# Performance work log

Measured on AMD Instinct MI355X. Metric: run time of the kernel, lower is better.

## Reference

```python
import jax, jax.numpy as jnp
import numpy as np

H = 256
VOCAB = 32000
B = 128
T = 2048


def setup_inputs() -> dict:
    key = jax.random.key(0)
    ks = jax.random.split(key, 14)
    s = 0.05
    return {
        "tokens": jax.random.randint(ks[0], (B, 1), 0, VOCAB),
        "hidden": jax.random.normal(ks[1], (1, B, H), jnp.float32),
        "encoder_outputs": jax.random.normal(ks[2], (T, B, H), jnp.float32),
        "emb_table": jax.random.normal(ks[3], (VOCAB + 1, H), jnp.float32) * s,
        "attn_W": jax.random.normal(ks[4], (1, 2 * H), jnp.float32) * s,
        "attn_b": jax.random.normal(ks[5], (1,), jnp.float32) * s,
        "comb_W": jax.random.normal(ks[6], (H, 2 * H), jnp.float32) * s,
        "comb_b": jax.random.normal(ks[7], (H,), jnp.float32) * s,
        "gru_Wih": jax.random.normal(ks[8], (3 * H, H), jnp.float32) * s,
        "gru_Whh": jax.random.normal(ks[9], (3 * H, H), jnp.float32) * s,
        "gru_bih": jax.random.normal(ks[10], (3 * H,), jnp.float32) * s,
        "gru_bhh": jax.random.normal(ks[11], (3 * H,), jnp.float32) * s,
        "out_W": jax.random.normal(ks[12], (VOCAB, H), jnp.float32) * s,
        "out_b": jax.random.normal(ks[13], (VOCAB,), jnp.float32) * s,
    }


def reference(tokens, hidden, encoder_outputs, emb_table, attn_W, attn_b,
              comb_W, comb_b, gru_Wih, gru_Whh, gru_bih, gru_bhh, out_W, out_b):
    h = hidden.shape[-1]
    # Embedding lookup: [B,1] -> [B,1,H] -> [1,B,H]
    emb = jnp.transpose(emb_table[tokens], (1, 0, 2))
    # Additive attention: Linear([hidden; enc_t]) -> scalar score per position.
    # attn_W splits into hidden part (first H cols) and encoder part (last H).
    W_h, W_e = attn_W[:, :h], attn_W[:, h:]          # [1,H] each
    scores = (jnp.einsum('tbh,oh->tbo', encoder_outputs, W_e)
              + jnp.einsum('lbh,oh->lbo', hidden, W_h)  # broadcast over T
              + attn_b)                                  # [T,B,1]
    attn_w = jax.nn.softmax(scores, axis=0)              # softmax over time
    # Context: weighted sum over time -> [1,B,H]
    ctx = jnp.einsum('tbo,tbh->obh', attn_w, encoder_outputs)
    # Combine embedded input with context, relu
    x = jnp.concatenate([emb, ctx], axis=2)              # [1,B,2H]
    x = jax.nn.relu(jnp.einsum('lbk,hk->lbh', x, comb_W) + comb_b)  # [1,B,H]
    # Single GRU step (PyTorch gate ordering: r, z, n)
    gx = x[0] @ gru_Wih.T + gru_bih                      # [B,3H]
    gh = hidden[0] @ gru_Whh.T + gru_bhh                 # [B,3H]
    r = jax.nn.sigmoid(gx[:, :h] + gh[:, :h])
    z = jax.nn.sigmoid(gx[:, h:2 * h] + gh[:, h:2 * h])
    n = jnp.tanh(gx[:, 2 * h:] + r * gh[:, 2 * h:])
    h_new = ((1.0 - z) * n + z * hidden[0])[None]        # [1,B,H]
    # Output projection + log_softmax over vocab
    logits = jnp.einsum('lbh,vh->lbv', h_new, out_W) + out_b
    logp = jax.nn.log_softmax(logits, axis=2)            # [1,B,V]
    return (logp, h_new, jnp.transpose(attn_w, (1, 0, 2)), ctx)
```

## Files before the change

### kernel.cpp

```cpp
#include <hip/hip_runtime.h>
#include <cstddef>

constexpr int H  = 256;
constexpr int Bb = 128;
constexpr int T  = 2048;
constexpr int V  = 32000;
constexpr int SPLITS = 16;
constexpr int TC = T / SPLITS;
constexpr int NPART = SPLITS * 4;
constexpr int LSE_SPLIT = 4;
constexpr int VS = V / LSE_SPLIT;

typedef __attribute__((ext_vector_type(8))) short short8;
typedef __attribute__((ext_vector_type(4))) float f32x4;

__device__ __forceinline__ unsigned short bf1(float a) {
  unsigned u = __builtin_bit_cast(unsigned, a);
  return (unsigned short)((u + 0x7fffu + ((u >> 16) & 1u)) >> 16);
}
__device__ __forceinline__ unsigned bfpack2(float a, float b) {
  unsigned ua = __builtin_bit_cast(unsigned, a);
  unsigned ub = __builtin_bit_cast(unsigned, b);
  ua = (ua + 0x7fffu + ((ua >> 16) & 1u)) >> 16;
  ub = (ub + 0x7fffu + ((ub >> 16) & 1u)) & 0xffff0000u;
  return ua | ub;
}

__global__ __launch_bounds__(256) void k_attn(
    const float* __restrict__ enc, const float* __restrict__ hidden,
    const float* __restrict__ attn_W, const float* __restrict__ attn_b,
    float* __restrict__ scores, float* __restrict__ ctx_part) {
  const int b = blockIdx.y, chunk = blockIdx.x;
  const int tid = threadIdx.x, lane = tid & 63, wave = tid >> 6;

  const float4 we = *(const float4*)(attn_W + H + lane * 4);
  const float4 wh = *(const float4*)(attn_W + lane * 4);
  const float4 hv = *(const float4*)(hidden + (size_t)b * H + lane * 4);

  float hb = fmaf(wh.x, hv.x, fmaf(wh.y, hv.y, fmaf(wh.z, hv.z, wh.w * hv.w)));
  #pragma unroll
  for (int off = 1; off < 64; off <<= 1) hb += __shfl_xor(hb, off);
  hb += attn_b[0];

  const int t0 = chunk * TC + wave * 32;
  const float* base = enc + (size_t)t0 * (Bb * H) + (size_t)b * H + lane * 4;

  float4 acc = {0.f, 0.f, 0.f, 0.f};
  for (int i = 0; i < 32; i += 4) {
    float4 e0 = *(const float4*)(base + (size_t)(i + 0) * (Bb * H));
    float4 e1 = *(const float4*)(base + (size_t)(i + 1) * (Bb * H));
    float4 e2 = *(const float4*)(base + (size_t)(i + 2) * (Bb * H));
    float4 e3 = *(const float4*)(base + (size_t)(i + 3) * (Bb * H));

    float p0 = fmaf(e0.x, we.x, fmaf(e0.y, we.y, fmaf(e0.z, we.z, e0.w * we.w)));
    float p1 = fmaf(e1.x, we.x, fmaf(e1.y, we.y, fmaf(e1.z, we.z, e1.w * we.w)));
    float p2 = fmaf(e2.x, we.x, fmaf(e2.y, we.y, fmaf(e2.z, we.z, e2.w * we.w)));
    float p3 = fmaf(e3.x, we.x, fmaf(e3.y, we.y, fmaf(e3.z, we.z, e3.w * we.w)));
    #pragma unroll
    for (int off = 1; off < 64; off <<= 1) {
      p0 += __shfl_xor(p0, off);
      p1 += __shfl_xor(p1, off);
      p2 += __shfl_xor(p2, off);
      p3 += __shfl_xor(p3, off);
    }
    float s0 = p0 + hb, s1 = p1 + hb, s2 = p2 + hb, s3 = p3 + hb;
    float w0 = __expf(s0), w1 = __expf(s1), w2 = __expf(s2), w3 = __expf(s3);

    acc.x = fmaf(w0, e0.x, fmaf(w1, e1.x, fmaf(w2, e2.x, fmaf(w3, e3.x, acc.x))));
    acc.y = fmaf(w0, e0.y, fmaf(w1, e1.y, fmaf(w2, e2.y, fmaf(w3, e3.y, acc.y))));
    acc.z = fmaf(w0, e0.z, fmaf(w1, e1.z, fmaf(w2, e2.z, fmaf(w3, e3.z, acc.z))));
    acc.w = fmaf(w0, e0.w, fmaf(w1, e1.w, fmaf(w2, e2.w, fmaf(w3, e3.w, acc.w))));

    if (lane == 0) {
      float4 sv = {s0, s1, s2, s3};
      *(float4*)(scores + (size_t)b * T + t0 + i) = sv;
    }
  }
  float* cp = ctx_part + ((size_t)b * NPART + chunk * 4 + wave) * H + lane * 4;
  *(float4*)cp = acc;
}

__global__ __launch_bounds__(256) void k_softmax_ctx(
    const float* __restrict__ scores, const float* __restrict__ ctx_part,
    float* __restrict__ attn_o, float* __restrict__ ctx_o) {
  const int b = blockIdx.x, tid = threadIdx.x;
  const int lane = tid & 63, wave = tid >> 6;
  __shared__ float red[4];
  __shared__ float m_sh, l_sh;

  const float* sb = scores + (size_t)b * T;
  float s[8];
  #pragma unroll
  for (int q = 0; q < 8; q++) s[q] = sb[tid + 256 * q];

  float mx = s[0];
  #pragma unroll
  for (int q = 1; q < 8; q++) mx = fmaxf(mx, s[q]);
  #pragma unroll
  for (int off = 1; off < 64; off <<= 1) mx = fmaxf(mx, __shfl_xor(mx, off));
  if (lane == 0) red[wave] = mx;
  __syncthreads();
  if (tid == 0) m_sh = fmaxf(fmaxf(red[0], red[1]), fmaxf(red[2], red[3]));
  __syncthreads();
  const float m = m_sh;

  float w[8];
  float ps = 0.f;
  #pragma unroll
  for (int q = 0; q < 8; q++) { w[q] = __expf(s[q] - m); ps += w[q]; }
  #pragma unroll
  for (int off = 1; off < 64; off <<= 1) ps += __shfl_xor(ps, off);
  __syncthreads();
  if (lane == 0) red[wave] = ps;
  __syncthreads();
  if (tid == 0) l_sh = red[0] + red[1] + red[2] + red[3];
  __syncthreads();
  const float inv = 1.f / l_sh;

  #pragma unroll
  for (int q = 0; q < 8; q++) attn_o[(size_t)b * T + tid + 256 * q] = w[q] * inv;

  float c = 0.f;
  for (int si = 0; si < NPART; si++)
    c += ctx_part[((size_t)b * NPART + si) * H + tid];
  ctx_o[(size_t)b * H + tid] = c * __expf(-m) * inv;
}

__global__ __launch_bounds__(256) void k_comb_gru(
    const int* __restrict__ tokens, const float* __restrict__ hidden,
    const float* __restrict__ emb_table,
    const float* __restrict__ comb_W, const float* __restrict__ comb_b,
    const float* __restrict__ Wih, const float* __restrict__ Whh,
    const float* __restrict__ bih, const float* __restrict__ bhh,
    const float* __restrict__ ctx_o, float* __restrict__ hnew,
    unsigned short* __restrict__ hnewb) {
  const int b = blockIdx.x, tid = threadIdx.x;
  __shared__ __align__(16) float x2[2 * H];
  __shared__ __align__(16) float hid[H];
  __shared__ __align__(16) float xs[H];

  const int tok = tokens[b];
  x2[tid]     = emb_table[(size_t)tok * H + tid];
  x2[H + tid] = ctx_o[(size_t)b * H + tid];
  hid[tid]    = hidden[(size_t)b * H + tid];
  __syncthreads();

  {
    const float4* wr = (const float4*)(comb_W + (size_t)tid * (2 * H));
    const float4* xr = (const float4*)x2;
    float a = 0.f;
    #pragma unroll 8
    for (int k = 0; k < (2 * H) / 4; k++) {
      float4 w = wr[k], x = xr[k];
      a += w.x * x.x + w.y * x.y + w.z * x.z + w.w * x.w;
    }
    a += comb_b[tid];
    xs[tid] = fmaxf(a, 0.f);
  }
  __syncthreads();

  auto dot256 = [](const float* __restrict__ row, const float* __restrict__ v) -> float {
    const float4* r4 = (const float4*)row;
    const float4* v4 = (const float4*)v;
    float a = 0.f;
    #pragma unroll 8
    for (int k = 0; k < H / 4; k++) {
      float4 w = r4[k], x = v4[k];
      a += w.x * x.x + w.y * x.y + w.z * x.z + w.w * x.w;
    }
    return a;
  };

  float gxr = dot256(Wih + (size_t)tid * H,           xs) + bih[tid];
  float gxz = dot256(Wih + (size_t)(tid + H) * H,     xs) + bih[tid + H];
  float gxn = dot256(Wih + (size_t)(tid + 2 * H) * H, xs) + bih[tid + 2 * H];
  float ghr = dot256(Whh + (size_t)tid * H,           hid) + bhh[tid];
  float ghz = dot256(Whh + (size_t)(tid + H) * H,     hid) + bhh[tid + H];
  float ghn = dot256(Whh + (size_t)(tid + 2 * H) * H, hid) + bhh[tid + 2 * H];

  float r = 1.f / (1.f + __expf(-(gxr + ghr)));
  float z = 1.f / (1.f + __expf(-(gxz + ghz)));
  float n = tanhf(gxn + r * ghn);
  float hv = (1.f - z) * n + z * hid[tid];
  hnew[(size_t)b * H + tid] = hv;
  hnewb[(size_t)b * H + tid] = bf1(hv);
}

constexpr int LSTR = 72;
__global__ __launch_bounds__(256) void k_logits(
    const unsigned short* __restrict__ hnewb, const float* __restrict__ out_W,
    const float* __restrict__ out_b, float* __restrict__ logits) {
  const int tid = threadIdx.x;
  const int lane = tid & 63, wave = tid >> 6;
  const int v0 = blockIdx.x * 128;
  const int r16 = lane & 15, quad = lane >> 4;

  __shared__ __align__(16) short lA[128 * LSTR];
  __shared__ __align__(16) short lB[128 * LSTR];

  f32x4 acc[8][2];
  #pragma unroll
  for (int mt = 0; mt < 8; mt++) {
    acc[mt][0] = (f32x4){0.f, 0.f, 0.f, 0.f};
    acc[mt][1] = (f32x4){0.f, 0.f, 0.f, 0.f};
  }

  for (int k0 = 0; k0 < H; k0 += 64) {
    #pragma unroll
    for (int q = 0; q < 4; q++) {
      int idx = q * 256 + tid;
      int row = idx >> 3, c8 = idx & 7;
      f32x4 v = *(const f32x4*)(hnewb + (size_t)row * H + k0 + c8 * 8);
      *(f32x4*)(&lA[row * LSTR + c8 * 8]) = v;
    }
    #pragma unroll
    for (int q = 0; q < 8; q++) {
      int idx = q * 256 + tid;
      int row = idx >> 4, c4 = idx & 15;
      f32x4 wv = *(const f32x4*)(out_W + (size_t)(v0 + row) * H + k0 + c4 * 4);
      uint2 p;
      p.x = bfpack2(wv.x, wv.y);
      p.y = bfpack2(wv.z, wv.w);
      *(uint2*)(&lB[row * LSTR + c4 * 4]) = p;
    }
    __syncthreads();
    #pragma unroll
    for (int ks = 0; ks < 2; ks++) {
      short8 bf[2];
      #pragma unroll
      for (int nt = 0; nt < 2; nt++) {
        int row = wave * 32 + nt * 16 + r16;
        bf[nt] = *(const short8*)(&lB[row * LSTR + ks * 32 + quad * 8]);
      }
      #pragma unroll
      for (int mt = 0; mt < 8; mt++) {
        short8 af = *(const short8*)(&lA[(mt * 16 + r16) * LSTR + ks * 32 + quad * 8]);
        acc[mt][0] = __builtin_amdgcn_mfma_f32_16x16x32_bf16(af, bf[0], acc[mt][0], 0, 0, 0);
        acc[mt][1] = __builtin_amdgcn_mfma_f32_16x16x32_bf16(af, bf[1], acc[mt][1], 0, 0, 0);
      }
    }
    __syncthreads();
  }

  #pragma unroll
  for (int nt = 0; nt < 2; nt++) {
    int col = v0 + wave * 32 + nt * 16 + r16;
    float bias = out_b[col];
    #pragma unroll
    for (int mt = 0; mt < 8; mt++) {
      int brow = mt * 16 + quad * 4;
      #pragma unroll
      for (int r = 0; r < 4; r++)
        logits[(size_t)(brow + r) * V + col] = acc[mt][nt][r] + bias;
    }
  }
}

__global__ __launch_bounds__(256) void k_lse(
    const float* __restrict__ logits, float2* __restrict__ lse_part) {
  const int b = blockIdx.x, s = blockIdx.y, tid = threadIdx.x;
  const int lane = tid & 63, wave = tid >> 6;
  const float4* base = (const float4*)(logits + (size_t)b * V + (size_t)s * VS);

  float4 m4 = {-1e30f, -1e30f, -1e30f, -1e30f};
  float4 l4 = {0.f, 0.f, 0.f, 0.f};
  for (int i = tid; i < VS / 4; i += 256) {
    float4 x = base[i];
    float nm;
    nm = fmaxf(m4.x, x.x); l4.x = l4.x * __expf(m4.x - nm) + __expf(x.x - nm); m4.x = nm;
    nm = fmaxf(m4.y, x.y); l4.y = l4.y * __expf(m4.y - nm) + __expf(x.y - nm); m4.y = nm;
    nm = fmaxf(m4.z, x.z); l4.z = l4.z * __expf(m4.z - nm) + __expf(x.z - nm); m4.z = nm;
    nm = fmaxf(m4.w, x.w); l4.w = l4.w * __expf(m4.w - nm) + __expf(x.w - nm); m4.w = nm;
  }
  float m = fmaxf(fmaxf(m4.x, m4.y), fmaxf(m4.z, m4.w));
  float l = l4.x * __expf(m4.x - m) + l4.y * __expf(m4.y - m) +
            l4.z * __expf(m4.z - m) + l4.w * __expf(m4.w - m);
  #pragma unroll
  for (int off = 1; off < 64; off <<= 1) {
    float mo = __shfl_xor(m, off), lo = __shfl_xor(l, off);
    float nm = fmaxf(m, mo);
    l = l * __expf(m - nm) + lo * __expf(mo - nm);
    m = nm;
  }
  __shared__ float sm[4], sl[4];
  if (lane == 0) { sm[wave] = m; sl[wave] = l; }
  __syncthreads();
  if (tid == 0) {
    float M = sm[0], L = sl[0];
    #pragma unroll
    for (int w2 = 1; w2 < 4; w2++) {
      float nm = fmaxf(M, sm[w2]);
      L = L * __expf(M - nm) + sl[w2] * __expf(sm[w2] - nm);
      M = nm;
    }
    lse_part[b * LSE_SPLIT + s] = make_float2(M, L);
  }
}

__global__ __launch_bounds__(256) void k_sub(
    float* __restrict__ logits, const float2* __restrict__ lse_part) {
  const int b = blockIdx.y;
  const int i = blockIdx.x * 256 + threadIdx.x;
  float2 p0 = lse_part[b * 4 + 0], p1 = lse_part[b * 4 + 1];
  float2 p2 = lse_part[b * 4 + 2], p3 = lse_part[b * 4 + 3];
  float M = fmaxf(fmaxf(p0.x, p1.x), fmaxf(p2.x, p3.x));
  float L = p0.y * __expf(p0.x - M) + p1.y * __expf(p1.x - M) +
            p2.y * __expf(p2.x - M) + p3.y * __expf(p3.x - M);
  float lse = M + logf(L);
  if (i < V / 4) {
    float4* p = (float4*)(logits + (size_t)b * V) + i;
    float4 x = *p;
    x.x -= lse; x.y -= lse; x.z -= lse; x.w -= lse;
    *p = x;
  }
}

extern "C" void kernel_launch(void* const* d_in, const int* in_sizes, int n_in,
                              void* d_out, int out_size, void* d_ws, size_t ws_size,
                              hipStream_t stream) {
  const int*   tokens = (const int*)d_in[0];
  const float* hidden = (const float*)d_in[1];
  const float* enc    = (const float*)d_in[2];
  const float* emb    = (const float*)d_in[3];
  const float* attn_W = (const float*)d_in[4];
  const float* attn_b = (const float*)d_in[5];
  const float* comb_W = (const float*)d_in[6];
  const float* comb_b = (const float*)d_in[7];
  const float* Wih    = (const float*)d_in[8];
  const float* Whh    = (const float*)d_in[9];
  const float* bih    = (const float*)d_in[10];
  const float* bhh    = (const float*)d_in[11];
  const float* out_W  = (const float*)d_in[12];
  const float* out_b  = (const float*)d_in[13];

  float* out    = (float*)d_out;
  float* logp   = out;
  float* hnew   = out + (size_t)Bb * V;
  float* attn_o = hnew + (size_t)Bb * H;
  float* ctx_o  = attn_o + (size_t)Bb * T;

  float* ws       = (float*)d_ws;
  float* scores   = ws;
  float* ctx_part = ws + (size_t)Bb * T;
  float2* lse_part = (float2*)(ctx_part + (size_t)Bb * NPART * H);
  unsigned short* hnewb = (unsigned short*)(lse_part + Bb * LSE_SPLIT);

  k_attn<<<dim3(SPLITS, Bb), 256, 0, stream>>>(enc, hidden, attn_W, attn_b, scores, ctx_part);
  k_softmax_ctx<<<dim3(Bb), 256, 0, stream>>>(scores, ctx_part, attn_o, ctx_o);
  k_comb_gru<<<dim3(Bb), 256, 0, stream>>>(tokens, hidden, emb, comb_W, comb_b,
                                           Wih, Whh, bih, bhh, ctx_o, hnew, hnewb);
  k_logits<<<dim3(V / 128), 256, 0, stream>>>(hnewb, out_W, out_b, logp);
  k_lse<<<dim3(Bb, LSE_SPLIT), 256, 0, stream>>>(logp, lse_part);
  k_sub<<<dim3(V / 1024 + 1, Bb), 256, 0, stream>>>(logp, lse_part);
}
```

Measured before the change: 507.7 us.

## Fuse softmax-ctx into GRU, compute LSE partials in logits epilogue

Merges the attention softmax/context kernel with the combine+GRU kernel and restructures the GRU matvecs so four lanes cooperate per output row, giving coalesced weight reads instead of one thread per row. The logits kernel now computes per-block max/sum-exp partials in its epilogue, so the separate pass that re-read the full logits tensor is replaced by a tiny finalize kernel over 250 partials per batch row. This removes one full read of the 16 MB logits buffer and a launch, at the cost of extra shuffles and shared memory in the GEMM epilogue. The lse partials reuse the scores workspace, which is safe because scores are consumed before k_logits runs.

```diff
diff --git a/kernel.cpp b/kernel.cpp
--- a/kernel.cpp
+++ b/kernel.cpp
@@ -8,8 +8,7 @@
 constexpr int SPLITS = 16;
 constexpr int TC = T / SPLITS;
 constexpr int NPART = SPLITS * 4;
-constexpr int LSE_SPLIT = 4;
-constexpr int VS = V / LSE_SPLIT;
+constexpr int NBLK = V / 128;
 
 typedef __attribute__((ext_vector_type(8))) short short8;
 typedef __attribute__((ext_vector_type(4))) float f32x4;
@@ -80,108 +79,134 @@
   *(float4*)cp = acc;
 }
 
-__global__ __launch_bounds__(256) void k_softmax_ctx(
+__global__ __launch_bounds__(256) void k_ctx_gru(
     const float* __restrict__ scores, const float* __restrict__ ctx_part,
-    float* __restrict__ attn_o, float* __restrict__ ctx_o) {
-  const int b = blockIdx.x, tid = threadIdx.x;
-  const int lane = tid & 63, wave = tid >> 6;
-  __shared__ float red[4];
-  __shared__ float m_sh, l_sh;
-
-  const float* sb = scores + (size_t)b * T;
-  float s[8];
-  #pragma unroll
-  for (int q = 0; q < 8; q++) s[q] = sb[tid + 256 * q];
-
-  float mx = s[0];
-  #pragma unroll
-  for (int q = 1; q < 8; q++) mx = fmaxf(mx, s[q]);
-  #pragma unroll
-  for (int off = 1; off < 64; off <<= 1) mx = fmaxf(mx, __shfl_xor(mx, off));
-  if (lane == 0) red[wave] = mx;
-  __syncthreads();
-  if (tid == 0) m_sh = fmaxf(fmaxf(red[0], red[1]), fmaxf(red[2], red[3]));
-  __syncthreads();
-  const float m = m_sh;
-
-  float w[8];
-  float ps = 0.f;
-  #pragma unroll
-  for (int q = 0; q < 8; q++) { w[q] = __expf(s[q] - m); ps += w[q]; }
-  #pragma unroll
-  for (int off = 1; off < 64; off <<= 1) ps += __shfl_xor(ps, off);
-  __syncthreads();
-  if (lane == 0) red[wave] = ps;
-  __syncthreads();
-  if (tid == 0) l_sh = red[0] + red[1] + red[2] + red[3];
-  __syncthreads();
-  const float inv = 1.f / l_sh;
-
-  #pragma unroll
-  for (int q = 0; q < 8; q++) attn_o[(size_t)b * T + tid + 256 * q] = w[q] * inv;
-
-  float c = 0.f;
-  for (int si = 0; si < NPART; si++)
-    c += ctx_part[((size_t)b * NPART + si) * H + tid];
-  ctx_o[(size_t)b * H + tid] = c * __expf(-m) * inv;
-}
-
-__global__ __launch_bounds__(256) void k_comb_gru(
+    float* __restrict__ attn_o, float* __restrict__ ctx_o,
     const int* __restrict__ tokens, const float* __restrict__ hidden,
     const float* __restrict__ emb_table,
     const float* __restrict__ comb_W, const float* __restrict__ comb_b,
     const float* __restrict__ Wih, const float* __restrict__ Whh,
     const float* __restrict__ bih, const float* __restrict__ bhh,
-    const float* __restrict__ ctx_o, float* __restrict__ hnew,
-    unsigned short* __restrict__ hnewb) {
+    float* __restrict__ hnew, unsigned short* __restrict__ hnewb) {
   const int b = blockIdx.x, tid = threadIdx.x;
+  const int lane = tid & 63, wave = tid >> 6;
+  const int g4 = lane >> 2, l4 = lane & 3;
+  __shared__ float red[4];
+  __shared__ float m_sh, l_sh;
   __shared__ __align__(16) float x2[2 * H];
   __shared__ __align__(16) float hid[H];
   __shared__ __align__(16) float xs[H];
-
-  const int tok = tokens[b];
-  x2[tid]     = emb_table[(size_t)tok * H + tid];
-  x2[H + tid] = ctx_o[(size_t)b * H + tid];
+  __shared__ float Ar[H], Az[H], Cn[H], Dn[H];
+
+  const float* sb = scores + (size_t)b * T;
+  float s[8];
+  #pragma unroll
+  for (int q = 0; q < 8; q++) s[q] = sb[tid + 256 * q];
+
+  float mx = s[0];
+  #pragma unroll
+  for (int q = 1; q < 8; q++) mx = fmaxf(mx, s[q]);
+  #pragma unroll
+  for (int off = 1; off < 64; off <<= 1) mx = fmaxf(mx, __shfl_xor(mx, off));
+  if (lane == 0) red[wave] = mx;
+  __syncthreads();
+  if (tid == 0) m_sh = fmaxf(fmaxf(red[0], red[1]), fmaxf(red[2], red[3]));
+  __syncthreads();
+  const float m = m_sh;
+
+  float w[8];
+  float ps = 0.f;
+  #pragma unroll
+  for (int q = 0; q < 8; q++) { w[q] = __expf(s[q] - m); ps += w[q]; }
+  #pragma unroll
+  for (int off = 1; off < 64; off <<= 1) ps += __shfl_xor(ps, off);
+  __syncthreads();
+  if (lane == 0) red[wave] = ps;
+  __syncthreads();
+  if (tid == 0) l_sh = red[0] + red[1] + red[2] + red[3];
+  __syncthreads();
+  const float inv = 1.f / l_sh;
+
+  #pragma unroll
+  for (int q = 0; q < 8; q++) attn_o[(size_t)b * T + tid + 256 * q] = w[q] * inv;
+
+  float c = 0.f;
+  for (int si = 0; si < NPART; si++)
+    c += ctx_part[((size_t)b * NPART + si) * H + tid];
+  const float cval = c * __expf(-m) * inv;
+  ctx_o[(size_t)b * H + tid] = cval;
+
+  x2[tid]     = emb_table[(size_t)tokens[b] * H + tid];
+  x2[H + tid] = cval;
   hid[tid]    = hidden[(size_t)b * H + tid];
   __syncthreads();
 
-  {
-    const float4* wr = (const float4*)(comb_W + (size_t)tid * (2 * H));
-    const float4* xr = (const float4*)x2;
-    float a = 0.f;
+  #pragma unroll 1
+  for (int batch = 0; batch < 4; batch++) {
+    const int row = wave * 64 + batch * 16 + g4;
+    const float* wr = comb_W + (size_t)row * (2 * H);
+    float p = 0.f;
     #pragma unroll 8
-    for (int k = 0; k < (2 * H) / 4; k++) {
-      float4 w = wr[k], x = xr[k];
-      a += w.x * x.x + w.y * x.y + w.z * x.z + w.w * x.w;
-    }
-    a += comb_b[tid];
-    xs[tid] = fmaxf(a, 0.f);
-  }
-  __syncthreads();
-
-  auto dot256 = [](const float* __restrict__ row, const float* __restrict__ v) -> float {
-    const float4* r4 = (const float4*)row;
-    const float4* v4 = (const float4*)v;
-    float a = 0.f;
-    #pragma unroll 8
-    for (int k = 0; k < H / 4; k++) {
-      float4 w = r4[k], x = v4[k];
-      a += w.x * x.x + w.y * x.y + w.z * x.z + w.w * x.w;
-    }
-    return a;
-  };
-
-  float gxr = dot256(Wih + (size_t)tid * H,           xs) + bih[tid];
-  float gxz = dot256(Wih + (size_t)(tid + H) * H,     xs) + bih[tid + H];
-  float gxn = dot256(Wih + (size_t)(tid + 2 * H) * H, xs) + bih[tid + 2 * H];
-  float ghr = dot256(Whh + (size_t)tid * H,           hid) + bhh[tid];
-  float ghz = dot256(Whh + (size_t)(tid + H) * H,     hid) + bhh[tid + H];
-  float ghn = dot256(Whh + (size_t)(tid + 2 * H) * H, hid) + bhh[tid + 2 * H];
-
-  float r = 1.f / (1.f + __expf(-(gxr + ghr)));
-  float z = 1.f / (1.f + __expf(-(gxz + ghz)));
-  float n = tanhf(gxn + r * ghn);
-  float hv = (1.f - z) * n + z * hid[tid];
+    for (int i = 0; i < 32; i++) {
+      const int o = i * 16 + l4 * 4;
+      float4 wv = *(const float4*)(wr + o);
+      float4 xv = *(const float4*)(x2 + o);
+      p = fmaf(wv.x, xv.x, fmaf(wv.y, xv.y, fmaf(wv.z, xv.z, fmaf(wv.w, xv.w, p))));
+    }
+    p += __shfl_xor(p, 1);
+    p += __shfl_xor(p, 2);
+    if (l4 == 0) xs[row] = fmaxf(p + comb_b[row], 0.f);
+  }
+  __syncthreads();
+
+  #pragma unroll 1
+  for (int batch = 0; batch < 4; batch++) {
+    const int row = wave * 64 + batch * 16 + g4;
+    const float* wxr = Wih + (size_t)row * H;
+    const float* wxz = Wih + (size_t)(row + H) * H;
+    const float* wxn = Wih + (size_t)(row + 2 * H) * H;
+    const float* whr = Whh + (size_t)row * H;
+    const float* whz = Whh + (size_t)(row + H) * H;
+    const float* whn = Whh + (size_t)(row + 2 * H) * H;
+    float pxr = 0.f, pxz = 0.f, pxn = 0.f, phr = 0.f, phz = 0.f, phn = 0.f;
+    #pragma unroll 2
+    for (int i = 0; i < 16; i++) {
+      const int o = i * 16 + l4 * 4;
+      float4 xv = *(const float4*)(xs + o);
+      float4 hv = *(const float4*)(hid + o);
+      float4 a;
+      a = *(const float4*)(wxr + o);
+      pxr = fmaf(a.x, xv.x, fmaf(a.y, xv.y, fmaf(a.z, xv.z, fmaf(a.w, xv.w, pxr))));
+      a = *(const float4*)(wxz + o);
+      pxz = fmaf(a.x, xv.x, fmaf(a.y, xv.y, fmaf(a.z, xv.z, fmaf(a.w, xv.w, pxz))));
+      a = *(const float4*)(wxn + o);
+      pxn = fmaf(a.x, xv.x, fmaf(a.y, xv.y, fmaf(a.z, xv.z, fmaf(a.w, xv.w, pxn))));
+      a = *(const float4*)(whr + o);
+      phr = fmaf(a.x, hv.x, fmaf(a.y, hv.y, fmaf(a.z, hv.z, fmaf(a.w, hv.w, phr))));
+      a = *(const float4*)(whz + o);
+      phz = fmaf(a.x, hv.x, fmaf(a.y, hv.y, fmaf(a.z, hv.z, fmaf(a.w, hv.w, phz))));
+      a = *(const float4*)(whn + o);
+      phn = fmaf(a.x, hv.x, fmaf(a.y, hv.y, fmaf(a.z, hv.z, fmaf(a.w, hv.w, phn))));
+    }
+    float sr = pxr + phr;
+    float sz = pxz + phz;
+    sr  += __shfl_xor(sr, 1);  sr  += __shfl_xor(sr, 2);
+    sz  += __shfl_xor(sz, 1);  sz  += __shfl_xor(sz, 2);
+    pxn += __shfl_xor(pxn, 1); pxn += __shfl_xor(pxn, 2);
+    phn += __shfl_xor(phn, 1); phn += __shfl_xor(phn, 2);
+    if (l4 == 0) {
+      Ar[row] = sr  + bih[row]         + bhh[row];
+      Az[row] = sz  + bih[row + H]     + bhh[row + H];
+      Cn[row] = pxn + bih[row + 2 * H];
+      Dn[row] = phn + bhh[row + 2 * H];
+    }
+  }
+  __syncthreads();
+
+  const float rg = 1.f / (1.f + __expf(-Ar[tid]));
+  const float zg = 1.f / (1.f + __expf(-Az[tid]));
+  const float ng = tanhf(Cn[tid] + rg * Dn[tid]);
+  const float hv = (1.f - zg) * ng + zg * hid[tid];
   hnew[(size_t)b * H + tid] = hv;
   hnewb[(size_t)b * H + tid] = bf1(hv);
 }
@@ -189,7 +214,8 @@
 constexpr int LSTR = 72;
 __global__ __launch_bounds__(256) void k_logits(
     const unsigned short* __restrict__ hnewb, const float* __restrict__ out_W,
-    const float* __restrict__ out_b, float* __restrict__ logits) {
+    const float* __restrict__ out_b, float* __restrict__ logits,
+    float2* __restrict__ lse_part) {
   const int tid = threadIdx.x;
   const int lane = tid & 63, wave = tid >> 6;
   const int v0 = blockIdx.x * 128;
@@ -197,6 +223,7 @@
 
   __shared__ __align__(16) short lA[128 * LSTR];
   __shared__ __align__(16) short lB[128 * LSTR];
+  __shared__ float2 lred[4][128];
 
   f32x4 acc[8][2];
   #pragma unroll
@@ -242,39 +269,51 @@
     __syncthreads();
   }
 
-  #pragma unroll
-  for (int nt = 0; nt < 2; nt++) {
-    int col = v0 + wave * 32 + nt * 16 + r16;
-    float bias = out_b[col];
-    #pragma unroll
-    for (int mt = 0; mt < 8; mt++) {
-      int brow = mt * 16 + quad * 4;
+  const int col0 = v0 + wave * 32 + r16;
+  const float bias0 = out_b[col0];
+  const float bias1 = out_b[col0 + 16];
+  #pragma unroll
+  for (int mt = 0; mt < 8; mt++) {
+    #pragma unroll
+    for (int r = 0; r < 4; r++) {
+      const int brow = mt * 16 + quad * 4 + r;
+      float a0 = acc[mt][0][r] + bias0;
+      float a1 = acc[mt][1][r] + bias1;
+      logits[(size_t)brow * V + col0]      = a0;
+      logits[(size_t)brow * V + col0 + 16] = a1;
+      float mv = fmaxf(a0, a1);
       #pragma unroll
-      for (int r = 0; r < 4; r++)
-        logits[(size_t)(brow + r) * V + col] = acc[mt][nt][r] + bias;
-    }
-  }
-}
-
-__global__ __launch_bounds__(256) void k_lse(
-    const float* __restrict__ logits, float2* __restrict__ lse_part) {
-  const int b = blockIdx.x, s = blockIdx.y, tid = threadIdx.x;
+      for (int off = 1; off < 16; off <<= 1) mv = fmaxf(mv, __shfl_xor(mv, off));
+      float lv = __expf(a0 - mv) + __expf(a1 - mv);
+      #pragma unroll
+      for (int off = 1; off < 16; off <<= 1) lv += __shfl_xor(lv, off);
+      if (r16 == 0) lred[wave][brow] = make_float2(mv, lv);
+    }
+  }
+  __syncthreads();
+  if (tid < 128) {
+    float2 p = lred[0][tid];
+    float M = p.x, L = p.y;
+    #pragma unroll
+    for (int w2 = 1; w2 < 4; w2++) {
+      float2 q = lred[w2][tid];
+      float nm = fmaxf(M, q.x);
+      L = L * __expf(M - nm) + q.y * __expf(q.x - nm);
+      M = nm;
+    }
+    lse_part[(size_t)tid * NBLK + blockIdx.x] = make_float2(M, L);
+  }
+}
+
+__global__ __launch_bounds__(256) void k_lsefin(
+    const float2* __restrict__ lse_part, float* __restrict__ lse) {
+  const int b = blockIdx.x, tid = threadIdx.x;
   const int lane = tid & 63, wave = tid >> 6;
-  const float4* base = (const float4*)(logits + (size_t)b * V + (size_t)s * VS);
-
-  float4 m4 = {-1e30f, -1e30f, -1e30f, -1e30f};
-  float4 l4 = {0.f, 0.f, 0.f, 0.f};
-  for (int i = tid; i < VS / 4; i += 256) {
-    float4 x = base[i];
-    float nm;
-    nm = fmaxf(m4.x, x.x); l4.x = l4.x * __expf(m4.x - nm) + __expf(x.x - nm); m4.x = nm;
-    nm = fmaxf(m4.y, x.y); l4.y = l4.y * __expf(m4.y - nm) + __expf(x.y - nm); m4.y = nm;
-    nm = fmaxf(m4.z, x.z); l4.z = l4.z * __expf(m4.z - nm) + __expf(x.z - nm); m4.z = nm;
-    nm = fmaxf(m4.w, x.w); l4.w = l4.w * __expf(m4.w - nm) + __expf(x.w - nm); m4.w = nm;
-  }
-  float m = fmaxf(fmaxf(m4.x, m4.y), fmaxf(m4.z, m4.w));
-  float l = l4.x * __expf(m4.x - m) + l4.y * __expf(m4.y - m) +
-            l4.z * __expf(m4.z - m) + l4.w * __expf(m4.w - m);
+  float m = -1e30f, l = 0.f;
+  if (tid < NBLK) {
+    float2 p = lse_part[(size_t)b * NBLK + tid];
+    m = p.x; l = p.y;
+  }
   #pragma unroll
   for (int off = 1; off < 64; off <<= 1) {
     float mo = __shfl_xor(m, off), lo = __shfl_xor(l, off);
@@ -293,24 +332,19 @@
       L = L * __expf(M - nm) + sl[w2] * __expf(sm[w2] - nm);
       M = nm;
     }
-    lse_part[b * LSE_SPLIT + s] = make_float2(M, L);
+    lse[b] = M + logf(L);
   }
 }
 
 __global__ __launch_bounds__(256) void k_sub(
-    float* __restrict__ logits, const float2* __restrict__ lse_part) {
+    float* __restrict__ logits, const float* __restrict__ lse) {
   const int b = blockIdx.y;
   const int i = blockIdx.x * 256 + threadIdx.x;
-  float2 p0 = lse_part[b * 4 + 0], p1 = lse_part[b * 4 + 1];
-  float2 p2 = lse_part[b * 4 + 2], p3 = lse_part[b * 4 + 3];
-  float M = fmaxf(fmaxf(p0.x, p1.x), fmaxf(p2.x, p3.x));
-  float L = p0.y * __expf(p0.x - M) + p1.y * __expf(p1.x - M) +
-            p2.y * __expf(p2.x - M) + p3.y * __expf(p3.x - M);
-  float lse = M + logf(L);
+  const float ls = lse[b];
   if (i < V / 4) {
     float4* p = (float4*)(logits + (size_t)b * V) + i;
     float4 x = *p;
-    x.x -= lse; x.y -= lse; x.z -= lse; x.w -= lse;
+    x.x -= ls; x.y -= ls; x.z -= ls; x.w -= ls;
     *p = x;
   }
 }
@@ -341,15 +375,16 @@
 
   float* ws       = (float*)d_ws;
   float* scores   = ws;
+  float2* lse_part = (float2*)ws;
   float* ctx_part = ws + (size_t)Bb * T;
-  float2* lse_part = (float2*)(ctx_part + (size_t)Bb * NPART * H);
-  unsigned short* hnewb = (unsigned short*)(lse_part + Bb * LSE_SPLIT);
+  unsigned short* hnewb = (unsigned short*)(ctx_part + (size_t)Bb * NPART * H);
+  float* lse      = (float*)(hnewb + (size_t)Bb * H);
 
   k_attn<<<dim3(SPLITS, Bb), 256, 0, stream>>>(enc, hidden, attn_W, attn_b, scores, ctx_part);
-  k_softmax_ctx<<<dim3(Bb), 256, 0, stream>>>(scores, ctx_part, attn_o, ctx_o);
-  k_comb_gru<<<dim3(Bb), 256, 0, stream>>>(tokens, hidden, emb, comb_W, comb_b,
-                                           Wih, Whh, bih, bhh, ctx_o, hnew, hnewb);
-  k_logits<<<dim3(V / 128), 256, 0, stream>>>(hnewb, out_W, out_b, logp);
-  k_lse<<<dim3(Bb, LSE_SPLIT), 256, 0, stream>>>(logp, lse_part);
-  k_sub<<<dim3(V / 1024 + 1, Bb), 256, 0, stream>>>(logp, lse_part);
-}
+  k_ctx_gru<<<dim3(Bb), 256, 0, stream>>>(scores, ctx_part, attn_o, ctx_o,
+                                          tokens, hidden, emb, comb_W, comb_b,
+                                          Wih, Whh, bih, bhh, hnew, hnewb);
+  k_logits<<<dim3(V / 128), 256, 0, stream>>>(hnewb, out_W, out_b, logp, lse_part);
+  k_lsefin<<<dim3(Bb), 256, 0, stream>>>(lse_part, lse);
+  k_sub<<<dim3(V / 1024 + 1, Bb), 256, 0, stream>>>(logp, lse);
+}
```

After: 499.7 us. Within noise of the previous version (-1.6%).
